# Kernel optimization log

Measured on AMD Instinct MI355X. Metric: run time of the kernel, lower is better.

The kernel has to match this reference:

```python
import jax, jax.numpy as jnp
import numpy as np

N_NODES = 100000
N_EDGES = 1600000
IN_FEATS = 128
HIDDEN = 128
NUM_CLASSES = 4


def setup_inputs() -> dict:
    key = jax.random.key(0)
    ks = jax.random.split(key, 8)
    features = jax.random.normal(ks[0], (N_NODES, IN_FEATS), dtype=jnp.float32)
    src = jax.random.randint(ks[1], (N_EDGES,), 0, N_NODES, dtype=jnp.int64)
    dst = jax.random.randint(ks[2], (N_EDGES,), 0, N_NODES, dtype=jnp.int64)
    s = 1.0 / np.sqrt(IN_FEATS)
    W1 = jax.random.normal(ks[3], (IN_FEATS, HIDDEN), dtype=jnp.float32) * s
    b1 = jnp.zeros((HIDDEN,), dtype=jnp.float32)
    W2 = jax.random.normal(ks[4], (HIDDEN, HIDDEN), dtype=jnp.float32) * s
    b2 = jnp.zeros((HIDDEN,), dtype=jnp.float32)
    Wc = jax.random.normal(ks[5], (HIDDEN, NUM_CLASSES), dtype=jnp.float32) * s
    bc = jnp.zeros((NUM_CLASSES,), dtype=jnp.float32)
    return {"features": features, "src": src, "dst": dst,
            "W1": W1, "b1": b1, "W2": W2, "b2": b2, "Wc": Wc, "bc": bc}


def _graph_conv(x, W, b, src, dst, n_nodes, activation=True):
    # DGL GraphConv, norm='both': D_out^{-1/2} A^T D_in... i.e. symmetric norm.
    ones = jnp.ones((src.shape[0],), dtype=x.dtype)
    deg_out = jnp.clip(jax.ops.segment_sum(ones, src, num_segments=n_nodes), 1.0)
    deg_in = jnp.clip(jax.ops.segment_sum(ones, dst, num_segments=n_nodes), 1.0)
    # scale sources, project (in >= out so matmul first, math-equivalent), gather-scatter
    h = (x * (deg_out ** -0.5)[:, None]) @ W            # [N, out]
    msg = h[src]                                         # [E, out] gather
    agg = jax.ops.segment_sum(msg, dst, num_segments=n_nodes)  # [N, out] scatter-add
    h = agg * (deg_in ** -0.5)[:, None] + b
    return jax.nn.relu(h) if activation else h


def reference(features, src, dst, W1, b1, W2, b2, Wc, bc):
    # eval-mode forward: dropout is identity
    n = features.shape[0]
    h = _graph_conv(features, W1, b1, src, dst, n, activation=True)
    h = _graph_conv(h, W2, b2, src, dst, n, activation=True)
    return h @ Wc + bc  # [N, num_classes] logits
```

## Files before the change

### kernel.cpp

```cpp
#include <hip/hip_runtime.h>
#include <hip/hip_fp16.h>
#include <math.h>

#define N_NODES 100000
#define N_EDGES 1600000
#define F 128
#define NBUK 196
#define BSH 9
#define BSZ 512
#define CAP 9216

typedef _Float16 half8 __attribute__((ext_vector_type(8)));
typedef _Float16 half4v __attribute__((ext_vector_type(4)));
typedef float    f32x4 __attribute__((ext_vector_type(4)));

__global__ __launch_bounds__(256) void init_pack(int* __restrict__ curD,
                                                 int* __restrict__ curS,
                                                 _Float16* __restrict__ padrow,
                                                 float* __restrict__ sout,
                                                 const float* __restrict__ W1,
                                                 const float* __restrict__ W2,
                                                 _Float16* __restrict__ hi1,
                                                 _Float16* __restrict__ lo1,
                                                 _Float16* __restrict__ hi2,
                                                 _Float16* __restrict__ lo2)
{
    int t = threadIdx.x;
    if (blockIdx.x == 0) {
        if (t < NBUK) { curD[t] = t * CAP; curS[t] = t * CAP; }
        if (t < 16) reinterpret_cast<int4*>(padrow)[t] = make_int4(0, 0, 0, 0);
        if (t == 255) sout[N_NODES] = 0.f;
        return;
    }
    int gidx = (blockIdx.x - 1) * 256 + t;
    const float* W = (gidx < 16384) ? W1 : W2;
    _Float16* hi = (gidx < 16384) ? hi1 : hi2;
    _Float16* lo = (gidx < 16384) ? lo1 : lo2;
    int idx = gidx & 16383;
    int f = idx >> 9, r = idx & 511;
    int l = r >> 3, j = r & 7;
    int kc = f >> 3, ct = f & 7;
    int k = kc * 32 + (l >> 4) * 8 + j;
    int n = ct * 16 + (l & 15);
    float w = W[k * 128 + n];
    _Float16 h = (_Float16)w;
    hi[idx] = h;
    lo[idx] = (_Float16)(w - (float)h);
}

__global__ __launch_bounds__(512) void part_gemm1(const int* __restrict__ src,
                                                  const int* __restrict__ dst,
                                                  int* __restrict__ curD,
                                                  int* __restrict__ curS,
                                                  int* __restrict__ bukD,
                                                  unsigned short* __restrict__ bukS,
                                                  const float* __restrict__ X,
                                                  const _Float16* __restrict__ Whi,
                                                  const _Float16* __restrict__ Wlo,
                                                  _Float16* __restrict__ Y, int N)
{
    __shared__ int hd[NBUK], hs[NBUK], bd[NBUK], bs[NBUK], cd[NBUK], cs[NBUK];
    const int tid = threadIdx.x;

    if (blockIdx.x < NBUK) {
        const int chunk = (((N_EDGES + NBUK - 1) / NBUK) + 3) & ~3;
        const int beg = blockIdx.x * chunk;
        const int end = min(beg + chunk, N_EDGES);
        if (beg >= end) return;
        if (tid < NBUK) { hd[tid] = 0; hs[tid] = 0; cd[tid] = 0; cs[tid] = 0; }
        __syncthreads();
        const int b4 = beg >> 2, e4 = end >> 2;
        for (int i = b4 + tid; i < e4; i += 512) {
            int4 d = reinterpret_cast<const int4*>(dst)[i];
            int4 s = reinterpret_cast<const int4*>(src)[i];
            atomicAdd(&hd[d.x >> BSH], 1); atomicAdd(&hd[d.y >> BSH], 1);
            atomicAdd(&hd[d.z >> BSH], 1); atomicAdd(&hd[d.w >> BSH], 1);
            atomicAdd(&hs[s.x >> BSH], 1); atomicAdd(&hs[s.y >> BSH], 1);
            atomicAdd(&hs[s.z >> BSH], 1); atomicAdd(&hs[s.w >> BSH], 1);
        }
        __syncthreads();
        if (tid < NBUK) {
            bd[tid] = hd[tid] ? atomicAdd(&curD[tid], hd[tid]) : 0;
            bs[tid] = hs[tid] ? atomicAdd(&curS[tid], hs[tid]) : 0;
        }
        __syncthreads();
        for (int e = beg + tid; e < end; e += 512) {
            int d = dst[e], s = src[e];
            int bin = d >> BSH;
            int r = atomicAdd(&cd[bin], 1);
            bukD[bd[bin] + r] = ((d & 511) << 17) | s;
            int bin2 = s >> BSH;
            int r2 = atomicAdd(&cs[bin2], 1);
            bukS[bs[bin2] + r2] = (unsigned short)(s & 511);
        }
        return;
    }

    const int l = tid & 63, w = tid >> 6;
    const int quad = l >> 4, m = l & 15;
    const int row0 = (blockIdx.x - NBUK) * 256;
    const half8* Bh = reinterpret_cast<const half8*>(Whi);
    const half8* Bl = reinterpret_cast<const half8*>(Wlo);

    f32x4 acc[2][8] = {};

    for (int kc = 0; kc < 4; kc++) {
        half8 ah[2];
        #pragma unroll
        for (int rt = 0; rt < 2; rt++) {
            int grow = row0 + w * 32 + rt * 16 + m;
            float4 xa = make_float4(0.f, 0.f, 0.f, 0.f), xb = xa;
            if (grow < N) {
                const float4* Xp = reinterpret_cast<const float4*>(X) + (size_t)grow * 32 + kc * 8 + quad * 2;
                xa = Xp[0]; xb = Xp[1];
            }
            ah[rt][0] = (_Float16)xa.x; ah[rt][1] = (_Float16)xa.y;
            ah[rt][2] = (_Float16)xa.z; ah[rt][3] = (_Float16)xa.w;
            ah[rt][4] = (_Float16)xb.x; ah[rt][5] = (_Float16)xb.y;
            ah[rt][6] = (_Float16)xb.z; ah[rt][7] = (_Float16)xb.w;
        }
        #pragma unroll
        for (int ct = 0; ct < 8; ct++) {
            int f = kc * 8 + ct;
            half8 bh = Bh[f * 64 + l];
            half8 bl = Bl[f * 64 + l];
            #pragma unroll
            for (int rt = 0; rt < 2; rt++) {
                acc[rt][ct] = __builtin_amdgcn_mfma_f32_16x16x32_f16(ah[rt], bh, acc[rt][ct], 0, 0, 0);
                acc[rt][ct] = __builtin_amdgcn_mfma_f32_16x16x32_f16(ah[rt], bl, acc[rt][ct], 0, 0, 0);
            }
        }
    }

    #pragma unroll
    for (int rt = 0; rt < 2; rt++) {
        #pragma unroll
        for (int r = 0; r < 4; r++) {
            int grow = row0 + w * 32 + rt * 16 + quad * 4 + r;
            if (grow < N) {
                #pragma unroll
                for (int ct = 0; ct < 8; ct++)
                    Y[(size_t)grow * 128 + ct * 16 + m] = (_Float16)(acc[rt][ct][r]);
            }
        }
    }
}

__global__ __launch_bounds__(512) void csr_deg(const int* __restrict__ bukD,
                                               const unsigned short* __restrict__ bukS,
                                               const int* __restrict__ curD,
                                               const int* __restrict__ curS,
                                               int* __restrict__ row_ptr,
                                               float* __restrict__ sin_,
                                               float* __restrict__ sout,
                                               int* __restrict__ col)
{
    __shared__ int h[BSZ], sc[BSZ], cur[BSZ];
    const int tid = threadIdx.x;

    if (blockIdx.x >= NBUK) {
        const int bid = blockIdx.x - NBUK;
        const int n0 = bid << BSH;
        const int lo = bid * CAP, hi = curS[bid];
        h[tid] = 0;
        __syncthreads();
        for (int i = lo + tid; i < hi; i += 512)
            atomicAdd(&h[bukS[i]], 1);
        __syncthreads();
        int node = n0 + tid;
        if (node < N_NODES) sout[node] = rsqrtf((float)max(h[tid], 1));
        return;
    }

    const int n0 = blockIdx.x << BSH;
    const int lo = blockIdx.x * CAP, hi = curD[blockIdx.x];
    h[tid] = 0;
    __syncthreads();
    for (int i = lo + tid; i < hi; i += 512)
        atomicAdd(&h[((unsigned)bukD[i]) >> 17], 1);
    __syncthreads();
    int own = h[tid];
    sc[tid] = own;
    __syncthreads();
    for (int off = 1; off < 512; off <<= 1) {
        int u = (tid >= off) ? sc[tid - off] : 0;
        __syncthreads();
        sc[tid] += u;
        __syncthreads();
    }
    int ex = sc[tid] - own;
    cur[tid] = ex;
    int node = n0 + tid;
    if (node < N_NODES) {
        row_ptr[2 * node]     = lo + ex;
        row_ptr[2 * node + 1] = lo + ex + own;
        sin_[node] = rsqrtf((float)max(own, 1));
    }
    __syncthreads();
    for (int i = lo + tid; i < hi; i += 512) {
        int p = bukD[i];
        int r = atomicAdd(&cur[((unsigned)p) >> 17], 1);
        col[lo + r] = p & 0x1FFFF;
    }
}

__global__ __launch_bounds__(256) void gather_agg_s(const _Float16* __restrict__ Hh,
                                                    const int* __restrict__ row_ptr,
                                                    const int* __restrict__ col,
                                                    const float* __restrict__ sout,
                                                    const float* __restrict__ sin_,
                                                    const float* __restrict__ bias,
                                                    _Float16* __restrict__ Yh, int N)
{
    int wave = blockIdx.x * 4 + (threadIdx.x >> 6);
    int lane = threadIdx.x & 63;
    int sub  = lane & 31;
    int node = wave * 2 + (lane >> 5);
    if (node >= N) return;
    int beg = row_ptr[2 * node], end = row_ptr[2 * node + 1];
    const half4v* H4 = reinterpret_cast<const half4v*>(Hh);
    float a0 = 0.f, a1 = 0.f, a2 = 0.f, a3 = 0.f;
    for (int i = beg; i < end; i += 4) {
        int c[4];
        #pragma unroll
        for (int j = 0; j < 4; j++)
            c[j] = (i + j < end) ? col[i + j] : N_NODES;
        float w[4];
        #pragma unroll
        for (int j = 0; j < 4; j++) w[j] = sout[c[j]];
        half4v v[4];
        #pragma unroll
        for (int j = 0; j < 4; j++)
            v[j] = H4[((size_t)c[j] << 5) | sub];
        #pragma unroll
        for (int j = 0; j < 4; j++) {
            a0 = fmaf(w[j], (float)v[j][0], a0);
            a1 = fmaf(w[j], (float)v[j][1], a1);
            a2 = fmaf(w[j], (float)v[j][2], a2);
            a3 = fmaf(w[j], (float)v[j][3], a3);
        }
    }
    float scn = sin_[node];
    float4 b = reinterpret_cast<const float4*>(bias)[sub];
    half4v o;
    o[0] = (_Float16)fmaxf(fmaf(a0, scn, b.x), 0.f);
    o[1] = (_Float16)fmaxf(fmaf(a1, scn, b.y), 0.f);
    o[2] = (_Float16)fmaxf(fmaf(a2, scn, b.z), 0.f);
    o[3] = (_Float16)fmaxf(fmaf(a3, scn, b.w), 0.f);
    reinterpret_cast<half4v*>(Yh)[((size_t)node << 5) | sub] = o;
}

__global__ __launch_bounds__(256) void gather_agg(const _Float16* __restrict__ Hh,
                                                  const int* __restrict__ row_ptr,
                                                  const int* __restrict__ col,
                                                  const float* __restrict__ sin_,
                                                  const float* __restrict__ bias,
                                                  _Float16* __restrict__ Yh, int N)
{
    int wave = blockIdx.x * 4 + (threadIdx.x >> 6);
    int lane = threadIdx.x & 63;
    int sub  = lane & 31;
    int node = wave * 2 + (lane >> 5);
    if (node >= N) return;
    int beg = row_ptr[2 * node], end = row_ptr[2 * node + 1];
    const half4v* H4 = reinterpret_cast<const half4v*>(Hh);
    float a0 = 0.f, a1 = 0.f, a2 = 0.f, a3 = 0.f;
    for (int i = beg; i < end; i += 4) {
        int c[4];
        #pragma unroll
        for (int j = 0; j < 4; j++)
            c[j] = (i + j < end) ? col[i + j] : N_NODES;
        half4v v[4];
        #pragma unroll
        for (int j = 0; j < 4; j++)
            v[j] = H4[((size_t)c[j] << 5) | sub];
        #pragma unroll
        for (int j = 0; j < 4; j++) {
            a0 += (float)v[j][0];
            a1 += (float)v[j][1];
            a2 += (float)v[j][2];
            a3 += (float)v[j][3];
        }
    }
    float scn = sin_[node];
    float4 b = reinterpret_cast<const float4*>(bias)[sub];
    half4v o;
    o[0] = (_Float16)fmaxf(fmaf(a0, scn, b.x), 0.f);
    o[1] = (_Float16)fmaxf(fmaf(a1, scn, b.y), 0.f);
    o[2] = (_Float16)fmaxf(fmaf(a2, scn, b.z), 0.f);
    o[3] = (_Float16)fmaxf(fmaf(a3, scn, b.w), 0.f);
    reinterpret_cast<half4v*>(Yh)[((size_t)node << 5) | sub] = o;
}

__global__ __launch_bounds__(256) void gemm_mfma_f16(const _Float16* __restrict__ Xh,
                                                     const _Float16* __restrict__ Whi,
                                                     const _Float16* __restrict__ Wlo,
                                                     const float* __restrict__ srow,
                                                     _Float16* __restrict__ Y, int N)
{
    const int tid = threadIdx.x;
    const int l = tid & 63, w = tid >> 6;
    const int quad = l >> 4, m = l & 15;
    const int row0 = blockIdx.x * 128;
    const half8* Bh = reinterpret_cast<const half8*>(Whi);
    const half8* Bl = reinterpret_cast<const half8*>(Wlo);

    f32x4 acc[2][8] = {};

    for (int kc = 0; kc < 4; kc++) {
        half8 a[2];
        #pragma unroll
        for (int rt = 0; rt < 2; rt++) {
            int grow = row0 + w * 32 + rt * 16 + m;
            half8 z = {};
            a[rt] = (grow < N)
                ? *reinterpret_cast<const half8*>(Xh + (size_t)grow * 128 + kc * 32 + quad * 8)
                : z;
        }
        #pragma unroll
        for (int ct = 0; ct < 8; ct++) {
            int f = kc * 8 + ct;
            half8 bh = Bh[f * 64 + l];
            half8 bl = Bl[f * 64 + l];
            #pragma unroll
            for (int rt = 0; rt < 2; rt++) {
                acc[rt][ct] = __builtin_amdgcn_mfma_f32_16x16x32_f16(a[rt], bh, acc[rt][ct], 0, 0, 0);
                acc[rt][ct] = __builtin_amdgcn_mfma_f32_16x16x32_f16(a[rt], bl, acc[rt][ct], 0, 0, 0);
            }
        }
    }

    #pragma unroll
    for (int rt = 0; rt < 2; rt++) {
        #pragma unroll
        for (int r = 0; r < 4; r++) {
            int grow = row0 + w * 32 + rt * 16 + quad * 4 + r;
            if (grow < N) {
                float s = srow[grow];
                #pragma unroll
                for (int ct = 0; ct < 8; ct++)
                    Y[(size_t)grow * 128 + ct * 16 + m] = (_Float16)(acc[rt][ct][r] * s);
            }
        }
    }
}

__global__ __launch_bounds__(256) void classifier(const __half* __restrict__ Hh,
                                                  const float* __restrict__ Wc,
                                                  const float* __restrict__ bc,
                                                  float* __restrict__ out, int N)
{
    __shared__ float4 Wcs[128];
    for (int i = threadIdx.x; i < 128; i += 256)
        Wcs[i] = reinterpret_cast<const float4*>(Wc)[i];
    __syncthreads();
    int i = blockIdx.x * 256 + threadIdx.x;
    if (i < N) {
        float4 acc = reinterpret_cast<const float4*>(bc)[0];
        const __half2* h2 = reinterpret_cast<const __half2*>(Hh) + (size_t)i * 64;
        #pragma unroll
        for (int j = 0; j < 64; j++) {
            float2 f = __half22float2(h2[j]);
            float4 w0 = Wcs[2 * j], w1 = Wcs[2 * j + 1];
            acc.x += f.x * w0.x + f.y * w1.x;
            acc.y += f.x * w0.y + f.y * w1.y;
            acc.z += f.x * w0.z + f.y * w1.z;
            acc.w += f.x * w0.w + f.y * w1.w;
        }
        reinterpret_cast<float4*>(out)[i] = acc;
    }
}

extern "C" void kernel_launch(void* const* d_in, const int* in_sizes, int n_in,
                              void* d_out, int out_size, void* d_ws, size_t ws_size,
                              hipStream_t stream)
{
    const float* features = (const float*)d_in[0];
    const int*   src      = (const int*)d_in[1];
    const int*   dst      = (const int*)d_in[2];
    const float* W1       = (const float*)d_in[3];
    const float* b1       = (const float*)d_in[4];
    const float* W2       = (const float*)d_in[5];
    const float* b2       = (const float*)d_in[6];
    const float* Wc       = (const float*)d_in[7];
    const float* bc       = (const float*)d_in[8];
    float* out = (float*)d_out;

    char* ws = (char*)d_ws;
    const size_t MB = 1 << 20;
    int* curD  = (int*)(ws + 0);
    int* curS  = (int*)(ws + 1024);
    float* sout    = (float*)(ws + 1 * MB);
    float* sin_    = (float*)(ws + 2 * MB);
    int*   row_ptr = (int*)(ws + 3 * MB);
    int*   col     = (int*)(ws + 4 * MB);
    int*   bukD    = (int*)(ws + 12 * MB);
    unsigned short* bukS = (unsigned short*)(ws + 20 * MB);
    _Float16* Whi1 = (_Float16*)(ws + 24 * MB);
    _Float16* Wlo1 = (_Float16*)(ws + 24 * MB + 32 * 1024);
    _Float16* Whi2 = (_Float16*)(ws + 24 * MB + 64 * 1024);
    _Float16* Wlo2 = (_Float16*)(ws + 24 * MB + 96 * 1024);
    _Float16* hMsg = (_Float16*)(ws + 25 * MB);
    _Float16* hA   = (_Float16*)(ws + 52 * MB);

    const int N = N_NODES;
    const int NGB = (N / 2 + 3) / 4;

    init_pack<<<129, 256, 0, stream>>>(curD, curS, hMsg + (size_t)N * F, sout,
                                       W1, W2, Whi1, Wlo1, Whi2, Wlo2);

    part_gemm1<<<NBUK + 391, 512, 0, stream>>>(src, dst, curD, curS, bukD, bukS,
                                               features, Whi1, Wlo1, hMsg, N);

    csr_deg<<<2 * NBUK, 512, 0, stream>>>(bukD, bukS, curD, curS,
                                          row_ptr, sin_, sout, col);

    gather_agg_s<<<NGB, 256, 0, stream>>>(hMsg, row_ptr, col, sout, sin_, b1, hA, N);

    gemm_mfma_f16<<<(N + 127) / 128, 256, 0, stream>>>(hA, Whi2, Wlo2, sout, hMsg, N);
    gather_agg<<<NGB, 256, 0, stream>>>(hMsg, row_ptr, col, sin_, b2, hA, N);

    classifier<<<(N + 255) / 256, 256, 0, stream>>>((const __half*)hA, Wc, bc, out, N);
}
```

Measured before the change: 328.0 us.

## Fuse classifier into second gather, precompute edge weights, use global out-degree atomics

Out-degrees are now counted with global atomics into a per-node array, which removes the source-bucket partition and its CSR pass. The CSR build pads each row to a multiple of 4 and writes a per-edge weight array next to the column indices. Both gather kernels now use 16 lanes per node with 8-wide half loads and vectorized col/weight reads. The classifier is fused into the second gather through a shuffle reduction, which drops one kernel launch and one round trip of the hidden features through memory. In exchange it adds global atomic contention, an extra weight array to read, and padding entries that point at a zero row.

```diff
diff --git a/kernel.cpp b/kernel.cpp
--- a/kernel.cpp
+++ b/kernel.cpp
@@ -8,16 +8,14 @@
 #define NBUK 196
 #define BSH 9
 #define BSZ 512
-#define CAP 9216
+#define CAP 10240
 
 typedef _Float16 half8 __attribute__((ext_vector_type(8)));
-typedef _Float16 half4v __attribute__((ext_vector_type(4)));
 typedef float    f32x4 __attribute__((ext_vector_type(4)));
 
 __global__ __launch_bounds__(256) void init_pack(int* __restrict__ curD,
-                                                 int* __restrict__ curS,
+                                                 int* __restrict__ degS,
                                                  _Float16* __restrict__ padrow,
-                                                 float* __restrict__ sout,
                                                  const float* __restrict__ W1,
                                                  const float* __restrict__ W2,
                                                  _Float16* __restrict__ hi1,
@@ -27,9 +25,13 @@
 {
     int t = threadIdx.x;
     if (blockIdx.x == 0) {
-        if (t < NBUK) { curD[t] = t * CAP; curS[t] = t * CAP; }
+        if (t < NBUK) curD[t] = t * CAP;
         if (t < 16) reinterpret_cast<int4*>(padrow)[t] = make_int4(0, 0, 0, 0);
-        if (t == 255) sout[N_NODES] = 0.f;
+        return;
+    }
+    if (blockIdx.x >= 129) {
+        int i = (blockIdx.x - 129) * 256 + t;
+        if (i < 25000) reinterpret_cast<int4*>(degS)[i] = make_int4(0, 0, 0, 0);
         return;
     }
     int gidx = (blockIdx.x - 1) * 256 + t;
@@ -51,15 +53,14 @@
 __global__ __launch_bounds__(512) void part_gemm1(const int* __restrict__ src,
                                                   const int* __restrict__ dst,
                                                   int* __restrict__ curD,
-                                                  int* __restrict__ curS,
+                                                  int* __restrict__ degS,
                                                   int* __restrict__ bukD,
-                                                  unsigned short* __restrict__ bukS,
                                                   const float* __restrict__ X,
                                                   const _Float16* __restrict__ Whi,
                                                   const _Float16* __restrict__ Wlo,
                                                   _Float16* __restrict__ Y, int N)
 {
-    __shared__ int hd[NBUK], hs[NBUK], bd[NBUK], bs[NBUK], cd[NBUK], cs[NBUK];
+    __shared__ int hd[NBUK], bd[NBUK], cd[NBUK];
     const int tid = threadIdx.x;
 
     if (blockIdx.x < NBUK) {
@@ -67,7 +68,7 @@
         const int beg = blockIdx.x * chunk;
         const int end = min(beg + chunk, N_EDGES);
         if (beg >= end) return;
-        if (tid < NBUK) { hd[tid] = 0; hs[tid] = 0; cd[tid] = 0; cs[tid] = 0; }
+        if (tid < NBUK) { hd[tid] = 0; cd[tid] = 0; }
         __syncthreads();
         const int b4 = beg >> 2, e4 = end >> 2;
         for (int i = b4 + tid; i < e4; i += 512) {
@@ -75,23 +76,18 @@
             int4 s = reinterpret_cast<const int4*>(src)[i];
             atomicAdd(&hd[d.x >> BSH], 1); atomicAdd(&hd[d.y >> BSH], 1);
             atomicAdd(&hd[d.z >> BSH], 1); atomicAdd(&hd[d.w >> BSH], 1);
-            atomicAdd(&hs[s.x >> BSH], 1); atomicAdd(&hs[s.y >> BSH], 1);
-            atomicAdd(&hs[s.z >> BSH], 1); atomicAdd(&hs[s.w >> BSH], 1);
+            atomicAdd(&degS[s.x], 1); atomicAdd(&degS[s.y], 1);
+            atomicAdd(&degS[s.z], 1); atomicAdd(&degS[s.w], 1);
         }
         __syncthreads();
-        if (tid < NBUK) {
+        if (tid < NBUK)
             bd[tid] = hd[tid] ? atomicAdd(&curD[tid], hd[tid]) : 0;
-            bs[tid] = hs[tid] ? atomicAdd(&curS[tid], hs[tid]) : 0;
-        }
         __syncthreads();
         for (int e = beg + tid; e < end; e += 512) {
             int d = dst[e], s = src[e];
             int bin = d >> BSH;
             int r = atomicAdd(&cd[bin], 1);
             bukD[bd[bin] + r] = ((d & 511) << 17) | s;
-            int bin2 = s >> BSH;
-            int r2 = atomicAdd(&cs[bin2], 1);
-            bukS[bs[bin2] + r2] = (unsigned short)(s & 511);
         }
         return;
     }
@@ -146,32 +142,16 @@
     }
 }
 
-__global__ __launch_bounds__(512) void csr_deg(const int* __restrict__ bukD,
-                                               const unsigned short* __restrict__ bukS,
-                                               const int* __restrict__ curD,
-                                               const int* __restrict__ curS,
-                                               int* __restrict__ row_ptr,
-                                               float* __restrict__ sin_,
-                                               float* __restrict__ sout,
-                                               int* __restrict__ col)
+__global__ __launch_bounds__(512) void csr_wv(const int* __restrict__ bukD,
+                                              const int* __restrict__ curD,
+                                              const int* __restrict__ degS,
+                                              int* __restrict__ row_ptr,
+                                              float* __restrict__ sin_,
+                                              int* __restrict__ col,
+                                              float* __restrict__ wv)
 {
     __shared__ int h[BSZ], sc[BSZ], cur[BSZ];
     const int tid = threadIdx.x;
-
-    if (blockIdx.x >= NBUK) {
-        const int bid = blockIdx.x - NBUK;
-        const int n0 = bid << BSH;
-        const int lo = bid * CAP, hi = curS[bid];
-        h[tid] = 0;
-        __syncthreads();
-        for (int i = lo + tid; i < hi; i += 512)
-            atomicAdd(&h[bukS[i]], 1);
-        __syncthreads();
-        int node = n0 + tid;
-        if (node < N_NODES) sout[node] = rsqrtf((float)max(h[tid], 1));
-        return;
-    }
-
     const int n0 = blockIdx.x << BSH;
     const int lo = blockIdx.x * CAP, hi = curD[blockIdx.x];
     h[tid] = 0;
@@ -180,7 +160,8 @@
         atomicAdd(&h[((unsigned)bukD[i]) >> 17], 1);
     __syncthreads();
     int own = h[tid];
-    sc[tid] = own;
+    int own4 = (own + 3) & ~3;
+    sc[tid] = own4;
     __syncthreads();
     for (int off = 1; off < 512; off <<= 1) {
         int u = (tid >= off) ? sc[tid - off] : 0;
@@ -188,114 +169,180 @@
         sc[tid] += u;
         __syncthreads();
     }
-    int ex = sc[tid] - own;
+    int ex = sc[tid] - own4;
     cur[tid] = ex;
     int node = n0 + tid;
     if (node < N_NODES) {
         row_ptr[2 * node]     = lo + ex;
-        row_ptr[2 * node + 1] = lo + ex + own;
+        row_ptr[2 * node + 1] = lo + ex + own4;
         sin_[node] = rsqrtf((float)max(own, 1));
     }
     __syncthreads();
     for (int i = lo + tid; i < hi; i += 512) {
         int p = bukD[i];
+        int s = p & 0x1FFFF;
         int r = atomicAdd(&cur[((unsigned)p) >> 17], 1);
-        col[lo + r] = p & 0x1FFFF;
-    }
-}
+        col[lo + r] = s;
+        wv[lo + r]  = rsqrtf((float)max(degS[s], 1));
+    }
+    for (int k = own; k < own4; k++) {
+        col[lo + ex + k] = N_NODES;
+        wv[lo + ex + k]  = 0.f;
+    }
+}
+
+#define ACCW(vv, ww) \
+    a0 = fmaf(ww, (float)vv[0], a0); a1 = fmaf(ww, (float)vv[1], a1); \
+    a2 = fmaf(ww, (float)vv[2], a2); a3 = fmaf(ww, (float)vv[3], a3); \
+    a4 = fmaf(ww, (float)vv[4], a4); a5 = fmaf(ww, (float)vv[5], a5); \
+    a6 = fmaf(ww, (float)vv[6], a6); a7 = fmaf(ww, (float)vv[7], a7);
+
+#define ACCU(vv) \
+    a0 += (float)vv[0]; a1 += (float)vv[1]; a2 += (float)vv[2]; a3 += (float)vv[3]; \
+    a4 += (float)vv[4]; a5 += (float)vv[5]; a6 += (float)vv[6]; a7 += (float)vv[7];
 
 __global__ __launch_bounds__(256) void gather_agg_s(const _Float16* __restrict__ Hh,
                                                     const int* __restrict__ row_ptr,
                                                     const int* __restrict__ col,
-                                                    const float* __restrict__ sout,
+                                                    const float* __restrict__ wv,
                                                     const float* __restrict__ sin_,
                                                     const float* __restrict__ bias,
                                                     _Float16* __restrict__ Yh, int N)
 {
-    int wave = blockIdx.x * 4 + (threadIdx.x >> 6);
-    int lane = threadIdx.x & 63;
-    int sub  = lane & 31;
-    int node = wave * 2 + (lane >> 5);
+    const int sub  = threadIdx.x & 15;
+    const int node = blockIdx.x * 16 + (threadIdx.x >> 4);
     if (node >= N) return;
-    int beg = row_ptr[2 * node], end = row_ptr[2 * node + 1];
-    const half4v* H4 = reinterpret_cast<const half4v*>(Hh);
-    float a0 = 0.f, a1 = 0.f, a2 = 0.f, a3 = 0.f;
-    for (int i = beg; i < end; i += 4) {
-        int c[4];
-        #pragma unroll
-        for (int j = 0; j < 4; j++)
-            c[j] = (i + j < end) ? col[i + j] : N_NODES;
-        float w[4];
-        #pragma unroll
-        for (int j = 0; j < 4; j++) w[j] = sout[c[j]];
-        half4v v[4];
-        #pragma unroll
-        for (int j = 0; j < 4; j++)
-            v[j] = H4[((size_t)c[j] << 5) | sub];
-        #pragma unroll
-        for (int j = 0; j < 4; j++) {
-            a0 = fmaf(w[j], (float)v[j][0], a0);
-            a1 = fmaf(w[j], (float)v[j][1], a1);
-            a2 = fmaf(w[j], (float)v[j][2], a2);
-            a3 = fmaf(w[j], (float)v[j][3], a3);
-        }
+    const int beg = row_ptr[2 * node], end = row_ptr[2 * node + 1];
+    const half8* __restrict__ H8 = reinterpret_cast<const half8*>(Hh);
+
+    float a0 = 0.f, a1 = 0.f, a2 = 0.f, a3 = 0.f, a4 = 0.f, a5 = 0.f, a6 = 0.f, a7 = 0.f;
+    int i = beg;
+    for (; i + 8 <= end; i += 8) {
+        int4 ca = *reinterpret_cast<const int4*>(col + i);
+        int4 cb = *reinterpret_cast<const int4*>(col + i + 4);
+        float4 wa = *reinterpret_cast<const float4*>(wv + i);
+        float4 wb = *reinterpret_cast<const float4*>(wv + i + 4);
+        half8 v0 = H8[((size_t)ca.x << 4) | sub];
+        half8 v1 = H8[((size_t)ca.y << 4) | sub];
+        half8 v2 = H8[((size_t)ca.z << 4) | sub];
+        half8 v3 = H8[((size_t)ca.w << 4) | sub];
+        half8 v4 = H8[((size_t)cb.x << 4) | sub];
+        half8 v5 = H8[((size_t)cb.y << 4) | sub];
+        half8 v6 = H8[((size_t)cb.z << 4) | sub];
+        half8 v7 = H8[((size_t)cb.w << 4) | sub];
+        ACCW(v0, wa.x) ACCW(v1, wa.y) ACCW(v2, wa.z) ACCW(v3, wa.w)
+        ACCW(v4, wb.x) ACCW(v5, wb.y) ACCW(v6, wb.z) ACCW(v7, wb.w)
+    }
+    if (i < end) {
+        int4 ca = *reinterpret_cast<const int4*>(col + i);
+        float4 wa = *reinterpret_cast<const float4*>(wv + i);
+        half8 v0 = H8[((size_t)ca.x << 4) | sub];
+        half8 v1 = H8[((size_t)ca.y << 4) | sub];
+        half8 v2 = H8[((size_t)ca.z << 4) | sub];
+        half8 v3 = H8[((size_t)ca.w << 4) | sub];
+        ACCW(v0, wa.x) ACCW(v1, wa.y) ACCW(v2, wa.z) ACCW(v3, wa.w)
     }
     float scn = sin_[node];
-    float4 b = reinterpret_cast<const float4*>(bias)[sub];
-    half4v o;
-    o[0] = (_Float16)fmaxf(fmaf(a0, scn, b.x), 0.f);
-    o[1] = (_Float16)fmaxf(fmaf(a1, scn, b.y), 0.f);
-    o[2] = (_Float16)fmaxf(fmaf(a2, scn, b.z), 0.f);
-    o[3] = (_Float16)fmaxf(fmaf(a3, scn, b.w), 0.f);
-    reinterpret_cast<half4v*>(Yh)[((size_t)node << 5) | sub] = o;
-}
-
-__global__ __launch_bounds__(256) void gather_agg(const _Float16* __restrict__ Hh,
+    const float4* B4 = reinterpret_cast<const float4*>(bias);
+    float4 bA = B4[2 * sub], bB = B4[2 * sub + 1];
+    half8 o;
+    o[0] = (_Float16)fmaxf(fmaf(a0, scn, bA.x), 0.f);
+    o[1] = (_Float16)fmaxf(fmaf(a1, scn, bA.y), 0.f);
+    o[2] = (_Float16)fmaxf(fmaf(a2, scn, bA.z), 0.f);
+    o[3] = (_Float16)fmaxf(fmaf(a3, scn, bA.w), 0.f);
+    o[4] = (_Float16)fmaxf(fmaf(a4, scn, bB.x), 0.f);
+    o[5] = (_Float16)fmaxf(fmaf(a5, scn, bB.y), 0.f);
+    o[6] = (_Float16)fmaxf(fmaf(a6, scn, bB.z), 0.f);
+    o[7] = (_Float16)fmaxf(fmaf(a7, scn, bB.w), 0.f);
+    reinterpret_cast<half8*>(Yh)[(size_t)node * 16 + sub] = o;
+}
+
+__global__ __launch_bounds__(256) void gather_cls(const _Float16* __restrict__ Hh,
                                                   const int* __restrict__ row_ptr,
                                                   const int* __restrict__ col,
                                                   const float* __restrict__ sin_,
                                                   const float* __restrict__ bias,
-                                                  _Float16* __restrict__ Yh, int N)
-{
-    int wave = blockIdx.x * 4 + (threadIdx.x >> 6);
-    int lane = threadIdx.x & 63;
-    int sub  = lane & 31;
-    int node = wave * 2 + (lane >> 5);
+                                                  const float* __restrict__ Wc,
+                                                  const float* __restrict__ bc,
+                                                  float* __restrict__ out, int N)
+{
+    __shared__ float4 Wcs[128];
+    for (int t = threadIdx.x; t < 128; t += 256)
+        Wcs[t] = reinterpret_cast<const float4*>(Wc)[t];
+    __syncthreads();
+
+    const int sub  = threadIdx.x & 15;
+    const int node = blockIdx.x * 16 + (threadIdx.x >> 4);
     if (node >= N) return;
-    int beg = row_ptr[2 * node], end = row_ptr[2 * node + 1];
-    const half4v* H4 = reinterpret_cast<const half4v*>(Hh);
-    float a0 = 0.f, a1 = 0.f, a2 = 0.f, a3 = 0.f;
-    for (int i = beg; i < end; i += 4) {
-        int c[4];
-        #pragma unroll
-        for (int j = 0; j < 4; j++)
-            c[j] = (i + j < end) ? col[i + j] : N_NODES;
-        half4v v[4];
-        #pragma unroll
-        for (int j = 0; j < 4; j++)
-            v[j] = H4[((size_t)c[j] << 5) | sub];
-        #pragma unroll
-        for (int j = 0; j < 4; j++) {
-            a0 += (float)v[j][0];
-            a1 += (float)v[j][1];
-            a2 += (float)v[j][2];
-            a3 += (float)v[j][3];
-        }
+    const int beg = row_ptr[2 * node], end = row_ptr[2 * node + 1];
+    const half8* __restrict__ H8 = reinterpret_cast<const half8*>(Hh);
+
+    float a0 = 0.f, a1 = 0.f, a2 = 0.f, a3 = 0.f, a4 = 0.f, a5 = 0.f, a6 = 0.f, a7 = 0.f;
+    int i = beg;
+    for (; i + 8 <= end; i += 8) {
+        int4 ca = *reinterpret_cast<const int4*>(col + i);
+        int4 cb = *reinterpret_cast<const int4*>(col + i + 4);
+        half8 v0 = H8[((size_t)ca.x << 4) | sub];
+        half8 v1 = H8[((size_t)ca.y << 4) | sub];
+        half8 v2 = H8[((size_t)ca.z << 4) | sub];
+        half8 v3 = H8[((size_t)ca.w << 4) | sub];
+        half8 v4 = H8[((size_t)cb.x << 4) | sub];
+        half8 v5 = H8[((size_t)cb.y << 4) | sub];
+        half8 v6 = H8[((size_t)cb.z << 4) | sub];
+        half8 v7 = H8[((size_t)cb.w << 4) | sub];
+        ACCU(v0) ACCU(v1) ACCU(v2) ACCU(v3)
+        ACCU(v4) ACCU(v5) ACCU(v6) ACCU(v7)
+    }
+    if (i < end) {
+        int4 ca = *reinterpret_cast<const int4*>(col + i);
+        half8 v0 = H8[((size_t)ca.x << 4) | sub];
+        half8 v1 = H8[((size_t)ca.y << 4) | sub];
+        half8 v2 = H8[((size_t)ca.z << 4) | sub];
+        half8 v3 = H8[((size_t)ca.w << 4) | sub];
+        ACCU(v0) ACCU(v1) ACCU(v2) ACCU(v3)
     }
     float scn = sin_[node];
-    float4 b = reinterpret_cast<const float4*>(bias)[sub];
-    half4v o;
-    o[0] = (_Float16)fmaxf(fmaf(a0, scn, b.x), 0.f);
-    o[1] = (_Float16)fmaxf(fmaf(a1, scn, b.y), 0.f);
-    o[2] = (_Float16)fmaxf(fmaf(a2, scn, b.z), 0.f);
-    o[3] = (_Float16)fmaxf(fmaf(a3, scn, b.w), 0.f);
-    reinterpret_cast<half4v*>(Yh)[((size_t)node << 5) | sub] = o;
+    const float4* B4 = reinterpret_cast<const float4*>(bias);
+    float4 bA = B4[2 * sub], bB = B4[2 * sub + 1];
+    float h0 = fmaxf(fmaf(a0, scn, bA.x), 0.f);
+    float h1 = fmaxf(fmaf(a1, scn, bA.y), 0.f);
+    float h2 = fmaxf(fmaf(a2, scn, bA.z), 0.f);
+    float h3 = fmaxf(fmaf(a3, scn, bA.w), 0.f);
+    float h4 = fmaxf(fmaf(a4, scn, bB.x), 0.f);
+    float h5 = fmaxf(fmaf(a5, scn, bB.y), 0.f);
+    float h6 = fmaxf(fmaf(a6, scn, bB.z), 0.f);
+    float h7 = fmaxf(fmaf(a7, scn, bB.w), 0.f);
+
+    float lx = 0.f, ly = 0.f, lz = 0.f, lw = 0.f;
+    float4 w;
+    w = Wcs[sub * 8 + 0]; lx = fmaf(h0, w.x, lx); ly = fmaf(h0, w.y, ly); lz = fmaf(h0, w.z, lz); lw = fmaf(h0, w.w, lw);
+    w = Wcs[sub * 8 + 1]; lx = fmaf(h1, w.x, lx); ly = fmaf(h1, w.y, ly); lz = fmaf(h1, w.z, lz); lw = fmaf(h1, w.w, lw);
+    w = Wcs[sub * 8 + 2]; lx = fmaf(h2, w.x, lx); ly = fmaf(h2, w.y, ly); lz = fmaf(h2, w.z, lz); lw = fmaf(h2, w.w, lw);
+    w = Wcs[sub * 8 + 3]; lx = fmaf(h3, w.x, lx); ly = fmaf(h3, w.y, ly); lz = fmaf(h3, w.z, lz); lw = fmaf(h3, w.w, lw);
+    w = Wcs[sub * 8 + 4]; lx = fmaf(h4, w.x, lx); ly = fmaf(h4, w.y, ly); lz = fmaf(h4, w.z, lz); lw = fmaf(h4, w.w, lw);
+    w = Wcs[sub * 8 + 5]; lx = fmaf(h5, w.x, lx); ly = fmaf(h5, w.y, ly); lz = fmaf(h5, w.z, lz); lw = fmaf(h5, w.w, lw);
+    w = Wcs[sub * 8 + 6]; lx = fmaf(h6, w.x, lx); ly = fmaf(h6, w.y, ly); lz = fmaf(h6, w.z, lz); lw = fmaf(h6, w.w, lw);
+    w = Wcs[sub * 8 + 7]; lx = fmaf(h7, w.x, lx); ly = fmaf(h7, w.y, ly); lz = fmaf(h7, w.z, lz); lw = fmaf(h7, w.w, lw);
+
+    #pragma unroll
+    for (int m = 1; m < 16; m <<= 1) {
+        lx += __shfl_xor(lx, m);
+        ly += __shfl_xor(ly, m);
+        lz += __shfl_xor(lz, m);
+        lw += __shfl_xor(lw, m);
+    }
+    if (sub == 0) {
+        float4 bcv = reinterpret_cast<const float4*>(bc)[0];
+        float4 r;
+        r.x = lx + bcv.x; r.y = ly + bcv.y; r.z = lz + bcv.z; r.w = lw + bcv.w;
+        reinterpret_cast<float4*>(out)[node] = r;
+    }
 }
 
 __global__ __launch_bounds__(256) void gemm_mfma_f16(const _Float16* __restrict__ Xh,
                                                      const _Float16* __restrict__ Whi,
                                                      const _Float16* __restrict__ Wlo,
-                                                     const float* __restrict__ srow,
+                                                     const int* __restrict__ degS,
                                                      _Float16* __restrict__ Y, int N)
 {
     const int tid = threadIdx.x;
@@ -336,38 +383,12 @@
         for (int r = 0; r < 4; r++) {
             int grow = row0 + w * 32 + rt * 16 + quad * 4 + r;
             if (grow < N) {
-                float s = srow[grow];
+                float s = rsqrtf((float)max(degS[grow], 1));
                 #pragma unroll
                 for (int ct = 0; ct < 8; ct++)
                     Y[(size_t)grow * 128 + ct * 16 + m] = (_Float16)(acc[rt][ct][r] * s);
             }
         }
-    }
-}
-
-__global__ __launch_bounds__(256) void classifier(const __half* __restrict__ Hh,
-                                                  const float* __restrict__ Wc,
-                                                  const float* __restrict__ bc,
-                                                  float* __restrict__ out, int N)
-{
-    __shared__ float4 Wcs[128];
-    for (int i = threadIdx.x; i < 128; i += 256)
-        Wcs[i] = reinterpret_cast<const float4*>(Wc)[i];
-    __syncthreads();
-    int i = blockIdx.x * 256 + threadIdx.x;
-    if (i < N) {
-        float4 acc = reinterpret_cast<const float4*>(bc)[0];
-        const __half2* h2 = reinterpret_cast<const __half2*>(Hh) + (size_t)i * 64;
-        #pragma unroll
-        for (int j = 0; j < 64; j++) {
-            float2 f = __half22float2(h2[j]);
-            float4 w0 = Wcs[2 * j], w1 = Wcs[2 * j + 1];
-            acc.x += f.x * w0.x + f.y * w1.x;
-            acc.y += f.x * w0.y + f.y * w1.y;
-            acc.z += f.x * w0.z + f.y * w1.z;
-            acc.w += f.x * w0.w + f.y * w1.w;
-        }
-        reinterpret_cast<float4*>(out)[i] = acc;
     }
 }
 
@@ -389,36 +410,32 @@
     char* ws = (char*)d_ws;
     const size_t MB = 1 << 20;
     int* curD  = (int*)(ws + 0);
-    int* curS  = (int*)(ws + 1024);
-    float* sout    = (float*)(ws + 1 * MB);
-    float* sin_    = (float*)(ws + 2 * MB);
-    int*   row_ptr = (int*)(ws + 3 * MB);
-    int*   col     = (int*)(ws + 4 * MB);
-    int*   bukD    = (int*)(ws + 12 * MB);
-    unsigned short* bukS = (unsigned short*)(ws + 20 * MB);
-    _Float16* Whi1 = (_Float16*)(ws + 24 * MB);
-    _Float16* Wlo1 = (_Float16*)(ws + 24 * MB + 32 * 1024);
-    _Float16* Whi2 = (_Float16*)(ws + 24 * MB + 64 * 1024);
-    _Float16* Wlo2 = (_Float16*)(ws + 24 * MB + 96 * 1024);
-    _Float16* hMsg = (_Float16*)(ws + 25 * MB);
+    _Float16* Whi1 = (_Float16*)(ws + 64 * 1024);
+    _Float16* Wlo1 = (_Float16*)(ws + 96 * 1024);
+    _Float16* Whi2 = (_Float16*)(ws + 128 * 1024);
+    _Float16* Wlo2 = (_Float16*)(ws + 160 * 1024);
+    int*   degS    = (int*)(ws + 512 * 1024);
+    float* sin_    = (float*)(ws + 1 * MB);
+    int*   row_ptr = (int*)(ws + 2 * MB);
+    int*   col     = (int*)(ws + 3 * MB);
+    float* wv      = (float*)(ws + 11 * MB);
+    int*   bukD    = (int*)(ws + 19 * MB);
+    _Float16* hMsg = (_Float16*)(ws + 27 * MB);
     _Float16* hA   = (_Float16*)(ws + 52 * MB);
 
     const int N = N_NODES;
-    const int NGB = (N / 2 + 3) / 4;
-
-    init_pack<<<129, 256, 0, stream>>>(curD, curS, hMsg + (size_t)N * F, sout,
+    const int NGB = (N + 15) / 16;
+
+    init_pack<<<227, 256, 0, stream>>>(curD, degS, hMsg + (size_t)N * F,
                                        W1, W2, Whi1, Wlo1, Whi2, Wlo2);
 
-    part_gemm1<<<NBUK + 391, 512, 0, stream>>>(src, dst, curD, curS, bukD, bukS,
+    part_gemm1<<<NBUK + 391, 512, 0, stream>>>(src, dst, curD, degS, bukD,
                                                features, Whi1, Wlo1, hMsg, N);
 
-    csr_deg<<<2 * NBUK, 512, 0, stream>>>(bukD, bukS, curD, curS,
-                                          row_ptr, sin_, sout, col);
-
-    gather_agg_s<<<NGB, 256, 0, stream>>>(hMsg, row_ptr, col, sout, sin_, b1, hA, N);
-
-    gemm_mfma_f16<<<(N + 127) / 128, 256, 0, stream>>>(hA, Whi2, Wlo2, sout, hMsg, N);
-    gather_agg<<<NGB, 256, 0, stream>>>(hMsg, row_ptr, col, sin_, b2, hA, N);
-
-    classifier<<<(N + 255) / 256, 256, 0, stream>>>((const __half*)hA, Wc, bc, out, N);
-}
+    csr_wv<<<NBUK, 512, 0, stream>>>(bukD, curD, degS, row_ptr, sin_, col, wv);
+
+    gather_agg_s<<<NGB, 256, 0, stream>>>(hMsg, row_ptr, col, wv, sin_, b1, hA, N);
+
+    gemm_mfma_f16<<<(N + 127) / 128, 256, 0, stream>>>(hA, Whi2, Wlo2, degS, hMsg, N);
+    gather_cls<<<NGB, 256, 0, stream>>>(hMsg, row_ptr, col, sin_, b2, Wc, bc, out, N);
+}
```

Result: slower. 351.1 us (+7.0%).
